# Kernel optimization log

Hardware: AMD Instinct MI355X
Metric: run time of the kernel (lower is better)

Reference implementation:

```python
import jax, jax.numpy as jnp
import numpy as np

NUM_HEADS = 16

def setup_inputs() -> dict:
    key = jax.random.key(0)
    ks = jax.random.split(key, 11)
    B, S, E, H, KV = 32, 4, 1024, NUM_HEADS, 4096
    d = E // H
    inp = {
        "x": jax.random.normal(ks[0], (B, S, E), dtype=jnp.float32),
        "cache_k": jax.random.normal(ks[1], (B, H, KV, d), dtype=jnp.float32),
        "cache_v": jax.random.normal(ks[2], (B, H, KV, d), dtype=jnp.float32),
        "Wq": jax.random.normal(ks[3], (E, E), dtype=jnp.float32) * (E ** -0.5),
        "bq": jax.random.normal(ks[4], (E,), dtype=jnp.float32) * 0.01,
        "Wk": jax.random.normal(ks[5], (E, E), dtype=jnp.float32) * (E ** -0.5),
        "bk": jax.random.normal(ks[6], (E,), dtype=jnp.float32) * 0.01,
        "Wv": jax.random.normal(ks[7], (E, E), dtype=jnp.float32) * (E ** -0.5),
        "bv": jax.random.normal(ks[8], (E,), dtype=jnp.float32) * 0.01,
        "Wo": jax.random.normal(ks[9], (E, E), dtype=jnp.float32) * (E ** -0.5),
        "bo": jax.random.normal(ks[10], (E,), dtype=jnp.float32) * 0.01,
    }
    return inp


def reference(x, cache_k, cache_v, Wq, bq, Wk, bk, Wv, bv, Wo, bo):
    B, S, E = x.shape
    H = NUM_HEADS
    d = E // H
    # torch Linear: y = x @ W.T + b
    def proj(W, b):
        return (x @ W.T + b).reshape(B, S, H, d).transpose(0, 2, 1, 3)  # [B,H,S,d]
    Q = proj(Wq, bq)
    K_new = proj(Wk, bk)
    V_new = proj(Wv, bv)
    K = jnp.concatenate([cache_k, K_new], axis=2)  # [B,H,KV+S,d]
    V = jnp.concatenate([cache_v, V_new], axis=2)
    scores = jnp.einsum("bhqd,bhkd->bhqk", Q, K) / jnp.sqrt(jnp.float32(d))
    attn = jax.nn.softmax(scores, axis=-1)
    out = jnp.einsum("bhqk,bhkd->bhqd", attn, V)  # [B,H,S,d]
    out = out.transpose(0, 2, 1, 3).reshape(B, S, E)
    return out @ Wo.T + bo
```

## Files before the change

kernel.cpp:

```cpp
#include <hip/hip_runtime.h>
#include <math.h>

#define B_   32
#define S_   4
#define H_   16
#define D_   64
#define E_   1024
#define KV_  4096
#define NBH  512
#define CS   512
#define NC   9
#define RECSZ 264

__global__ __launch_bounds__(256) void proj_kernel(
    const float* __restrict__ A, const float* __restrict__ W,
    const float* __restrict__ bias, float* __restrict__ out, int mode) {
    __shared__ float a_lds[4 * E_];
    __shared__ float res[256];
    const int t0 = blockIdx.x * 4;
    const int n0 = blockIdx.y * 64;
    const int tid = threadIdx.x;
    const int lane = tid & 63, wid = tid >> 6;
    const int sub = lane >> 4, cg = lane & 15, tsel = cg & 3;

    const float4* Ag = (const float4*)(A + (size_t)t0 * E_);
    float4* al = (float4*)a_lds;
    #pragma unroll
    for (int i = 0; i < 4; ++i) al[tid + 256 * i] = Ag[tid + 256 * i];
    __syncthreads();

    #pragma unroll
    for (int g = 0; g < 4; ++g) {
        const int r0 = n0 + wid * 16 + g * 4;
        const float4* wrow = (const float4*)(W + (size_t)r0 * E_);
        float ac0 = 0.f, ac1 = 0.f, ac2 = 0.f, ac3 = 0.f;
        #pragma unroll
        for (int kk = 0; kk < 16; ++kk) {
            float4 w4 = wrow[sub * 256 + kk * 16 + cg];
            float4 a0 = *(const float4*)&a_lds[0 * E_ + kk * 64 + cg * 4];
            float4 a1 = *(const float4*)&a_lds[1 * E_ + kk * 64 + cg * 4];
            float4 a2 = *(const float4*)&a_lds[2 * E_ + kk * 64 + cg * 4];
            float4 a3 = *(const float4*)&a_lds[3 * E_ + kk * 64 + cg * 4];
            ac0 += w4.x * a0.x + w4.y * a0.y + w4.z * a0.z + w4.w * a0.w;
            ac1 += w4.x * a1.x + w4.y * a1.y + w4.z * a1.z + w4.w * a1.w;
            ac2 += w4.x * a2.x + w4.y * a2.y + w4.z * a2.z + w4.w * a2.w;
            ac3 += w4.x * a3.x + w4.y * a3.y + w4.z * a3.z + w4.w * a3.w;
        }
        ac0 += __shfl_xor(ac0, 1); ac0 += __shfl_xor(ac0, 2);
        ac1 += __shfl_xor(ac1, 1); ac1 += __shfl_xor(ac1, 2);
        ac2 += __shfl_xor(ac2, 1); ac2 += __shfl_xor(ac2, 2);
        ac3 += __shfl_xor(ac3, 1); ac3 += __shfl_xor(ac3, 2);
        float v = (tsel & 1) ? ((tsel & 2) ? ac3 : ac1)
                             : ((tsel & 2) ? ac2 : ac0);
        v += __shfl_xor(v, 4); v += __shfl_xor(v, 8);
        if (cg < 4) res[cg * 64 + (wid * 16 + g * 4 + sub)] = v;
    }
    __syncthreads();

    const float val = res[tid] + bias[n0 + (tid & 63)];
    const int t = t0 + (tid >> 6), e = n0 + (tid & 63);
    if (mode == 0) {
        const int b = t >> 2, s = t & 3, h = e >> 6, dk = e & 63;
        out[((size_t)((b * H_ + h) * S_ + s)) * D_ + dk] = val;
    } else {
        out[(size_t)t * E_ + e] = val;
    }
}

__device__ __forceinline__ float wave_max64(float v) {
    #pragma unroll
    for (int off = 32; off > 0; off >>= 1) v = fmaxf(v, __shfl_xor(v, off));
    return v;
}

__global__ __launch_bounds__(256) void attn_partial_kernel(
    const float* __restrict__ Qw, const float* __restrict__ Kc,
    const float* __restrict__ Vc, const float* __restrict__ Kn,
    const float* __restrict__ Vn, float* __restrict__ part) {
    __shared__ float q_s[S_ * D_];
    __shared__ float ob[4][256];
    __shared__ float mw[4];
    __shared__ float lw[4][4];

    const int bh = blockIdx.x;
    const int c = blockIdx.y;
    const int tid = threadIdx.x;
    const int lane = tid & 63, wid = tid >> 6;
    const int sub = lane >> 4, cg = lane & 15, qsel = cg & 3;

    q_s[tid] = Qw[(size_t)bh * 256 + tid];
    __syncthreads();

    const float* kptr;
    const float* vptr;
    int nrows;
    if (c < 8) {
        kptr = Kc + ((size_t)bh * KV_ + c * CS) * D_;
        vptr = Vc + ((size_t)bh * KV_ + c * CS) * D_;
        nrows = CS;
    } else {
        kptr = Kn + (size_t)bh * 256;
        vptr = Vn + (size_t)bh * 256;
        nrows = S_;
    }

    const float4 q0 = *(const float4*)&q_s[0 * 64 + cg * 4];
    const float4 q1 = *(const float4*)&q_s[1 * 64 + cg * 4];
    const float4 q2 = *(const float4*)&q_s[2 * 64 + cg * 4];
    const float4 q3 = *(const float4*)&q_s[3 * 64 + cg * 4];

    const float4 z4 = make_float4(0.f, 0.f, 0.f, 0.f);
    float m_run = -INFINITY;
    float l_run = 0.f;
    float4 a0 = z4, a1 = z4, a2 = z4, a3 = z4;

    int r0 = wid * 8;
    float4 kvA = z4, vvA = z4, kvB = z4, vvB = z4;
    bool vB = false;
    if (r0 < nrows) {
        kvA = ((const float4*)(kptr + (size_t)r0 * D_))[lane];
        vvA = ((const float4*)(vptr + (size_t)r0 * D_))[lane];
        if (r0 + 4 < nrows) {
            vB = true;
            kvB = ((const float4*)(kptr + (size_t)(r0 + 4) * D_))[lane];
            vvB = ((const float4*)(vptr + (size_t)(r0 + 4) * D_))[lane];
        }
    }

    while (r0 < nrows) {
        const int rn = r0 + 32;
        float4 nkA = z4, nvA = z4, nkB = z4, nvB = z4;
        bool vBn = false;
        if (rn < nrows) {
            nkA = ((const float4*)(kptr + (size_t)rn * D_))[lane];
            nvA = ((const float4*)(vptr + (size_t)rn * D_))[lane];
            if (rn + 4 < nrows) {
                vBn = true;
                nkB = ((const float4*)(kptr + (size_t)(rn + 4) * D_))[lane];
                nvB = ((const float4*)(vptr + (size_t)(rn + 4) * D_))[lane];
            }
        }

        float pA0 = kvA.x * q0.x + kvA.y * q0.y + kvA.z * q0.z + kvA.w * q0.w;
        float pA1 = kvA.x * q1.x + kvA.y * q1.y + kvA.z * q1.z + kvA.w * q1.w;
        float pA2 = kvA.x * q2.x + kvA.y * q2.y + kvA.z * q2.z + kvA.w * q2.w;
        float pA3 = kvA.x * q3.x + kvA.y * q3.y + kvA.z * q3.z + kvA.w * q3.w;
        float pB0 = kvB.x * q0.x + kvB.y * q0.y + kvB.z * q0.z + kvB.w * q0.w;
        float pB1 = kvB.x * q1.x + kvB.y * q1.y + kvB.z * q1.z + kvB.w * q1.w;
        float pB2 = kvB.x * q2.x + kvB.y * q2.y + kvB.z * q2.z + kvB.w * q2.w;
        float pB3 = kvB.x * q3.x + kvB.y * q3.y + kvB.z * q3.z + kvB.w * q3.w;

        pA0 += __shfl_xor(pA0, 1); pA0 += __shfl_xor(pA0, 2);
        pA1 += __shfl_xor(pA1, 1); pA1 += __shfl_xor(pA1, 2);
        pA2 += __shfl_xor(pA2, 1); pA2 += __shfl_xor(pA2, 2);
        pA3 += __shfl_xor(pA3, 1); pA3 += __shfl_xor(pA3, 2);
        pB0 += __shfl_xor(pB0, 1); pB0 += __shfl_xor(pB0, 2);
        pB1 += __shfl_xor(pB1, 1); pB1 += __shfl_xor(pB1, 2);
        pB2 += __shfl_xor(pB2, 1); pB2 += __shfl_xor(pB2, 2);
        pB3 += __shfl_xor(pB3, 1); pB3 += __shfl_xor(pB3, 2);

        float sA = (qsel & 1) ? ((qsel & 2) ? pA3 : pA1)
                              : ((qsel & 2) ? pA2 : pA0);
        float sB = (qsel & 1) ? ((qsel & 2) ? pB3 : pB1)
                              : ((qsel & 2) ? pB2 : pB0);
        sA += __shfl_xor(sA, 4); sA += __shfl_xor(sA, 8);
        sB += __shfl_xor(sB, 4); sB += __shfl_xor(sB, 8);
        sA *= 0.125f;
        sB = vB ? sB * 0.125f : -INFINITY;

        const float smax = fmaxf(sA, sB);
        if (__any(smax > m_run + 8.f)) {
            const float vmax = wave_max64(smax);
            const float newm = fmaxf(m_run, vmax);
            const float scale = __expf(m_run - newm);
            a0.x *= scale; a0.y *= scale; a0.z *= scale; a0.w *= scale;
            a1.x *= scale; a1.y *= scale; a1.z *= scale; a1.w *= scale;
            a2.x *= scale; a2.y *= scale; a2.z *= scale; a2.w *= scale;
            a3.x *= scale; a3.y *= scale; a3.z *= scale; a3.w *= scale;
            l_run *= scale;
            m_run = newm;
        }
        const float pxA = __expf(sA - m_run);
        const float pxB = __expf(sB - m_run);
        l_run += (cg < 4) ? (pxA + pxB) : 0.f;

        const int srcbase = (sub << 4);
        const float pa0 = __shfl(pxA, srcbase + 0);
        const float pa1 = __shfl(pxA, srcbase + 1);
        const float pa2 = __shfl(pxA, srcbase + 2);
        const float pa3 = __shfl(pxA, srcbase + 3);
        const float pb0 = __shfl(pxB, srcbase + 0);
        const float pb1 = __shfl(pxB, srcbase + 1);
        const float pb2 = __shfl(pxB, srcbase + 2);
        const float pb3 = __shfl(pxB, srcbase + 3);

        a0.x = fmaf(pa0, vvA.x, a0.x); a0.y = fmaf(pa0, vvA.y, a0.y);
        a0.z = fmaf(pa0, vvA.z, a0.z); a0.w = fmaf(pa0, vvA.w, a0.w);
        a1.x = fmaf(pa1, vvA.x, a1.x); a1.y = fmaf(pa1, vvA.y, a1.y);
        a1.z = fmaf(pa1, vvA.z, a1.z); a1.w = fmaf(pa1, vvA.w, a1.w);
        a2.x = fmaf(pa2, vvA.x, a2.x); a2.y = fmaf(pa2, vvA.y, a2.y);
        a2.z = fmaf(pa2, vvA.z, a2.z); a2.w = fmaf(pa2, vvA.w, a2.w);
        a3.x = fmaf(pa3, vvA.x, a3.x); a3.y = fmaf(pa3, vvA.y, a3.y);
        a3.z = fmaf(pa3, vvA.z, a3.z); a3.w = fmaf(pa3, vvA.w, a3.w);

        a0.x = fmaf(pb0, vvB.x, a0.x); a0.y = fmaf(pb0, vvB.y, a0.y);
        a0.z = fmaf(pb0, vvB.z, a0.z); a0.w = fmaf(pb0, vvB.w, a0.w);
        a1.x = fmaf(pb1, vvB.x, a1.x); a1.y = fmaf(pb1, vvB.y, a1.y);
        a1.z = fmaf(pb1, vvB.z, a1.z); a1.w = fmaf(pb1, vvB.w, a1.w);
        a2.x = fmaf(pb2, vvB.x, a2.x); a2.y = fmaf(pb2, vvB.y, a2.y);
        a2.z = fmaf(pb2, vvB.z, a2.z); a2.w = fmaf(pb2, vvB.w, a2.w);
        a3.x = fmaf(pb3, vvB.x, a3.x); a3.y = fmaf(pb3, vvB.y, a3.y);
        a3.z = fmaf(pb3, vvB.z, a3.z); a3.w = fmaf(pb3, vvB.w, a3.w);

        kvA = nkA; vvA = nvA; kvB = nkB; vvB = nvB; vB = vBn;
        r0 = rn;
    }

    a0.x += __shfl_xor(a0.x, 16); a0.x += __shfl_xor(a0.x, 32);
    a0.y += __shfl_xor(a0.y, 16); a0.y += __shfl_xor(a0.y, 32);
    a0.z += __shfl_xor(a0.z, 16); a0.z += __shfl_xor(a0.z, 32);
    a0.w += __shfl_xor(a0.w, 16); a0.w += __shfl_xor(a0.w, 32);
    a1.x += __shfl_xor(a1.x, 16); a1.x += __shfl_xor(a1.x, 32);
    a1.y += __shfl_xor(a1.y, 16); a1.y += __shfl_xor(a1.y, 32);
    a1.z += __shfl_xor(a1.z, 16); a1.z += __shfl_xor(a1.z, 32);
    a1.w += __shfl_xor(a1.w, 16); a1.w += __shfl_xor(a1.w, 32);
    a2.x += __shfl_xor(a2.x, 16); a2.x += __shfl_xor(a2.x, 32);
    a2.y += __shfl_xor(a2.y, 16); a2.y += __shfl_xor(a2.y, 32);
    a2.z += __shfl_xor(a2.z, 16); a2.z += __shfl_xor(a2.z, 32);
    a2.w += __shfl_xor(a2.w, 16); a2.w += __shfl_xor(a2.w, 32);
    a3.x += __shfl_xor(a3.x, 16); a3.x += __shfl_xor(a3.x, 32);
    a3.y += __shfl_xor(a3.y, 16); a3.y += __shfl_xor(a3.y, 32);
    a3.z += __shfl_xor(a3.z, 16); a3.z += __shfl_xor(a3.z, 32);
    a3.w += __shfl_xor(a3.w, 16); a3.w += __shfl_xor(a3.w, 32);

    float l2 = l_run;
    l2 += __shfl_xor(l2, 16); l2 += __shfl_xor(l2, 32);

    if (sub == 0) {
        *(float4*)&ob[wid][0 * 64 + cg * 4] = a0;
        *(float4*)&ob[wid][1 * 64 + cg * 4] = a1;
        *(float4*)&ob[wid][2 * 64 + cg * 4] = a2;
        *(float4*)&ob[wid][3 * 64 + cg * 4] = a3;
    }
    if (lane < 4) lw[wid][lane] = l2;
    if (lane == 0) mw[wid] = m_run;
    __syncthreads();

    const float M = fmaxf(fmaxf(mw[0], mw[1]), fmaxf(mw[2], mw[3]));
    const float w0 = __expf(mw[0] - M), w1 = __expf(mw[1] - M);
    const float w2 = __expf(mw[2] - M), w3 = __expf(mw[3] - M);

    float* rec = part + ((size_t)bh * NC + c) * RECSZ;
    rec[8 + tid] = w0 * ob[0][tid] + w1 * ob[1][tid] +
                   w2 * ob[2][tid] + w3 * ob[3][tid];
    if (tid < 4) {
        rec[tid] = M;
        rec[4 + tid] = w0 * lw[0][tid] + w1 * lw[1][tid] +
                       w2 * lw[2][tid] + w3 * lw[3][tid];
    }
}

__global__ __launch_bounds__(256) void attn_combine_kernel(
    const float* __restrict__ part, float* __restrict__ attn_out) {
    const int bh = blockIdx.x;
    const int tid = threadIdx.x;
    const int q = tid >> 6, dl = tid & 63;
    const float* base = part + (size_t)bh * NC * RECSZ;

    float m = -1e30f;
    #pragma unroll
    for (int c = 0; c < NC; ++c) m = fmaxf(m, base[c * RECSZ + q]);
    float l = 0.f, o = 0.f;
    #pragma unroll
    for (int c = 0; c < NC; ++c) {
        float w = __expf(base[c * RECSZ + q] - m);
        l = fmaf(base[c * RECSZ + 4 + q], w, l);
        o = fmaf(base[c * RECSZ + 8 + tid], w, o);
    }
    const float res = o / l;
    const int b = bh >> 4, h = bh & 15;
    attn_out[((size_t)(b * S_ + q)) * E_ + h * D_ + dl] = res;
}

extern "C" void kernel_launch(void* const* d_in, const int* in_sizes, int n_in,
                              void* d_out, int out_size, void* d_ws, size_t ws_size,
                              hipStream_t stream) {
    const float* x  = (const float*)d_in[0];
    const float* ck = (const float*)d_in[1];
    const float* cv = (const float*)d_in[2];
    const float* Wq = (const float*)d_in[3];
    const float* bq = (const float*)d_in[4];
    const float* Wk = (const float*)d_in[5];
    const float* bk = (const float*)d_in[6];
    const float* Wv = (const float*)d_in[7];
    const float* bv = (const float*)d_in[8];
    const float* Wo = (const float*)d_in[9];
    const float* bo = (const float*)d_in[10];
    float* out = (float*)d_out;
    float* ws = (float*)d_ws;

    float* Qw = ws;
    float* Kn = ws + 131072;
    float* Vn = ws + 262144;
    float* part = ws + 393216;
    float* attn_out = ws + 393216 + 1216512;

    dim3 pg(32, 16), pb(256);
    hipLaunchKernelGGL(proj_kernel, pg, pb, 0, stream, x, Wq, bq, Qw, 0);
    hipLaunchKernelGGL(proj_kernel, pg, pb, 0, stream, x, Wk, bk, Kn, 0);
    hipLaunchKernelGGL(proj_kernel, pg, pb, 0, stream, x, Wv, bv, Vn, 0);
    hipLaunchKernelGGL(attn_partial_kernel, dim3(NBH, NC), dim3(256), 0, stream,
                       Qw, ck, cv, Kn, Vn, part);
    hipLaunchKernelGGL(attn_combine_kernel, dim3(NBH), dim3(256), 0, stream,
                       part, attn_out);
    hipLaunchKernelGGL(proj_kernel, pg, pb, 0, stream, attn_out, Wo, bo, out, 1);
}
```

Baseline: 251.2 us.

## Fuse QKV projections into one launch and merge combine with output projection

Batches the three Q/K/V projections into a single 3D-grid launch and folds the split-KV combine step into the output projection kernel, so the attention output never round-trips through global memory. This cuts the launch count from six to three. The GEMM core also now issues all four weight-row loads per k step in one loop, for more memory-level parallelism. In exchange, each of the 16 output-projection column blocks per batch recomputes the combine from the partials, which adds redundant reads and exp work.

```diff
diff --git a/kernel.cpp b/kernel.cpp
--- a/kernel.cpp
+++ b/kernel.cpp
@@ -12,40 +12,57 @@
 #define NC   9
 #define RECSZ 264
 
-__global__ __launch_bounds__(256) void proj_kernel(
-    const float* __restrict__ A, const float* __restrict__ W,
-    const float* __restrict__ bias, float* __restrict__ out, int mode) {
-    __shared__ float a_lds[4 * E_];
-    __shared__ float res[256];
-    const int t0 = blockIdx.x * 4;
-    const int n0 = blockIdx.y * 64;
-    const int tid = threadIdx.x;
+__device__ __forceinline__ void gemm_core(const float* __restrict__ a_lds,
+                                          const float* __restrict__ W,
+                                          int n0, int tid,
+                                          float* __restrict__ res) {
     const int lane = tid & 63, wid = tid >> 6;
     const int sub = lane >> 4, cg = lane & 15, tsel = cg & 3;
 
-    const float4* Ag = (const float4*)(A + (size_t)t0 * E_);
-    float4* al = (float4*)a_lds;
-    #pragma unroll
-    for (int i = 0; i < 4; ++i) al[tid + 256 * i] = Ag[tid + 256 * i];
-    __syncthreads();
+    float acc[4][4];
+    #pragma unroll
+    for (int g = 0; g < 4; ++g)
+        #pragma unroll
+        for (int t = 0; t < 4; ++t) acc[g][t] = 0.f;
+
+    const float4* wr0 = (const float4*)(W + (size_t)(n0 + wid * 16 + 0) * E_);
+    const float4* wr1 = (const float4*)(W + (size_t)(n0 + wid * 16 + 4) * E_);
+    const float4* wr2 = (const float4*)(W + (size_t)(n0 + wid * 16 + 8) * E_);
+    const float4* wr3 = (const float4*)(W + (size_t)(n0 + wid * 16 + 12) * E_);
+
+    #pragma unroll
+    for (int kk = 0; kk < 16; ++kk) {
+        const float4 a0 = *(const float4*)&a_lds[0 * E_ + kk * 64 + cg * 4];
+        const float4 a1 = *(const float4*)&a_lds[1 * E_ + kk * 64 + cg * 4];
+        const float4 a2 = *(const float4*)&a_lds[2 * E_ + kk * 64 + cg * 4];
+        const float4 a3 = *(const float4*)&a_lds[3 * E_ + kk * 64 + cg * 4];
+        const int wi = sub * 256 + kk * 16 + cg;
+        float4 w;
+        w = wr0[wi];
+        acc[0][0] += w.x*a0.x + w.y*a0.y + w.z*a0.z + w.w*a0.w;
+        acc[0][1] += w.x*a1.x + w.y*a1.y + w.z*a1.z + w.w*a1.w;
+        acc[0][2] += w.x*a2.x + w.y*a2.y + w.z*a2.z + w.w*a2.w;
+        acc[0][3] += w.x*a3.x + w.y*a3.y + w.z*a3.z + w.w*a3.w;
+        w = wr1[wi];
+        acc[1][0] += w.x*a0.x + w.y*a0.y + w.z*a0.z + w.w*a0.w;
+        acc[1][1] += w.x*a1.x + w.y*a1.y + w.z*a1.z + w.w*a1.w;
+        acc[1][2] += w.x*a2.x + w.y*a2.y + w.z*a2.z + w.w*a2.w;
+        acc[1][3] += w.x*a3.x + w.y*a3.y + w.z*a3.z + w.w*a3.w;
+        w = wr2[wi];
+        acc[2][0] += w.x*a0.x + w.y*a0.y + w.z*a0.z + w.w*a0.w;
+        acc[2][1] += w.x*a1.x + w.y*a1.y + w.z*a1.z + w.w*a1.w;
+        acc[2][2] += w.x*a2.x + w.y*a2.y + w.z*a2.z + w.w*a2.w;
+        acc[2][3] += w.x*a3.x + w.y*a3.y + w.z*a3.z + w.w*a3.w;
+        w = wr3[wi];
+        acc[3][0] += w.x*a0.x + w.y*a0.y + w.z*a0.z + w.w*a0.w;
+        acc[3][1] += w.x*a1.x + w.y*a1.y + w.z*a1.z + w.w*a1.w;
+        acc[3][2] += w.x*a2.x + w.y*a2.y + w.z*a2.z + w.w*a2.w;
+        acc[3][3] += w.x*a3.x + w.y*a3.y + w.z*a3.z + w.w*a3.w;
+    }
 
     #pragma unroll
     for (int g = 0; g < 4; ++g) {
-        const int r0 = n0 + wid * 16 + g * 4;
-        const float4* wrow = (const float4*)(W + (size_t)r0 * E_);
-        float ac0 = 0.f, ac1 = 0.f, ac2 = 0.f, ac3 = 0.f;
-        #pragma unroll
-        for (int kk = 0; kk < 16; ++kk) {
-            float4 w4 = wrow[sub * 256 + kk * 16 + cg];
-            float4 a0 = *(const float4*)&a_lds[0 * E_ + kk * 64 + cg * 4];
-            float4 a1 = *(const float4*)&a_lds[1 * E_ + kk * 64 + cg * 4];
-            float4 a2 = *(const float4*)&a_lds[2 * E_ + kk * 64 + cg * 4];
-            float4 a3 = *(const float4*)&a_lds[3 * E_ + kk * 64 + cg * 4];
-            ac0 += w4.x * a0.x + w4.y * a0.y + w4.z * a0.z + w4.w * a0.w;
-            ac1 += w4.x * a1.x + w4.y * a1.y + w4.z * a1.z + w4.w * a1.w;
-            ac2 += w4.x * a2.x + w4.y * a2.y + w4.z * a2.z + w4.w * a2.w;
-            ac3 += w4.x * a3.x + w4.y * a3.y + w4.z * a3.z + w4.w * a3.w;
-        }
+        float ac0 = acc[g][0], ac1 = acc[g][1], ac2 = acc[g][2], ac3 = acc[g][3];
         ac0 += __shfl_xor(ac0, 1); ac0 += __shfl_xor(ac0, 2);
         ac1 += __shfl_xor(ac1, 1); ac1 += __shfl_xor(ac1, 2);
         ac2 += __shfl_xor(ac2, 1); ac2 += __shfl_xor(ac2, 2);
@@ -55,16 +72,38 @@
         v += __shfl_xor(v, 4); v += __shfl_xor(v, 8);
         if (cg < 4) res[cg * 64 + (wid * 16 + g * 4 + sub)] = v;
     }
+}
+
+__global__ __launch_bounds__(256) void proj_qkv_kernel(
+    const float* __restrict__ x,
+    const float* __restrict__ Wq, const float* __restrict__ bq,
+    const float* __restrict__ Wk, const float* __restrict__ bk,
+    const float* __restrict__ Wv, const float* __restrict__ bv,
+    float* __restrict__ outbase) {
+    __shared__ float a_lds[4 * E_];
+    __shared__ float res[256];
+    const int t0 = blockIdx.x * 4;
+    const int n0 = blockIdx.y * 64;
+    const int z = blockIdx.z;
+    const int tid = threadIdx.x;
+
+    const float* W    = (z == 0) ? Wq : (z == 1) ? Wk : Wv;
+    const float* bias = (z == 0) ? bq : (z == 1) ? bk : bv;
+    float* out = outbase + (size_t)z * (B_ * S_ * E_);
+
+    const float4* Ag = (const float4*)(x + (size_t)t0 * E_);
+    float4* al = (float4*)a_lds;
+    #pragma unroll
+    for (int i = 0; i < 4; ++i) al[tid + 256 * i] = Ag[tid + 256 * i];
+    __syncthreads();
+
+    gemm_core(a_lds, W, n0, tid, res);
     __syncthreads();
 
     const float val = res[tid] + bias[n0 + (tid & 63)];
     const int t = t0 + (tid >> 6), e = n0 + (tid & 63);
-    if (mode == 0) {
-        const int b = t >> 2, s = t & 3, h = e >> 6, dk = e & 63;
-        out[((size_t)((b * H_ + h) * S_ + s)) * D_ + dk] = val;
-    } else {
-        out[(size_t)t * E_ + e] = val;
-    }
+    const int b = t >> 2, s = t & 3, h = e >> 6, dk = e & 63;
+    out[((size_t)((b * H_ + h) * S_ + s)) * D_ + dk] = val;
 }
 
 __device__ __forceinline__ float wave_max64(float v) {
@@ -260,26 +299,62 @@
     }
 }
 
-__global__ __launch_bounds__(256) void attn_combine_kernel(
-    const float* __restrict__ part, float* __restrict__ attn_out) {
-    const int bh = blockIdx.x;
+__global__ __launch_bounds__(256) void combine_proj_out_kernel(
+    const float* __restrict__ part, const float* __restrict__ Wo,
+    const float* __restrict__ bo, float* __restrict__ out) {
+    __shared__ float a_lds[4 * E_];
+    __shared__ float res[256];
+    __shared__ float wcoef[64][NC + 1];
+    __shared__ float linv[64];
+    const int b = blockIdx.x;
+    const int n0 = blockIdx.y * 64;
     const int tid = threadIdx.x;
-    const int q = tid >> 6, dl = tid & 63;
-    const float* base = part + (size_t)bh * NC * RECSZ;
-
-    float m = -1e30f;
-    #pragma unroll
-    for (int c = 0; c < NC; ++c) m = fmaxf(m, base[c * RECSZ + q]);
-    float l = 0.f, o = 0.f;
-    #pragma unroll
-    for (int c = 0; c < NC; ++c) {
-        float w = __expf(base[c * RECSZ + q] - m);
-        l = fmaf(base[c * RECSZ + 4 + q], w, l);
-        o = fmaf(base[c * RECSZ + 8 + tid], w, o);
-    }
-    const float res = o / l;
-    const int b = bh >> 4, h = bh & 15;
-    attn_out[((size_t)(b * S_ + q)) * E_ + h * D_ + dl] = res;
+
+    if (tid < 64) {
+        const int h = tid >> 2, s = tid & 3;
+        const float* base = part + ((size_t)(b * H_ + h) * NC) * RECSZ;
+        float m = -1e30f;
+        #pragma unroll
+        for (int c = 0; c < NC; ++c) m = fmaxf(m, base[c * RECSZ + s]);
+        float l = 0.f;
+        #pragma unroll
+        for (int c = 0; c < NC; ++c) {
+            const float w = __expf(base[c * RECSZ + s] - m);
+            wcoef[tid][c] = w;
+            l = fmaf(base[c * RECSZ + 4 + s], w, l);
+        }
+        linv[tid] = 1.f / l;
+    }
+    __syncthreads();
+
+    float4* al4 = (float4*)a_lds;
+    #pragma unroll
+    for (int i = 0; i < 4; ++i) {
+        const int idx = tid + 256 * i;
+        const int s = idx >> 8;
+        const int rest = idx & 255;
+        const int h = rest >> 4, dkg = rest & 15;
+        const float* base = part + ((size_t)(b * H_ + h) * NC) * RECSZ
+                          + 8 + s * 64 + dkg * 4;
+        float4 o = make_float4(0.f, 0.f, 0.f, 0.f);
+        #pragma unroll
+        for (int c = 0; c < NC; ++c) {
+            const float4 v = *(const float4*)(base + c * RECSZ);
+            const float w = wcoef[h * 4 + s][c];
+            o.x = fmaf(w, v.x, o.x); o.y = fmaf(w, v.y, o.y);
+            o.z = fmaf(w, v.z, o.z); o.w = fmaf(w, v.w, o.w);
+        }
+        const float li = linv[h * 4 + s];
+        o.x *= li; o.y *= li; o.z *= li; o.w *= li;
+        al4[idx] = o;
+    }
+    __syncthreads();
+
+    gemm_core(a_lds, Wo, n0, tid, res);
+    __syncthreads();
+
+    out[(size_t)(b * 4 + (tid >> 6)) * E_ + n0 + (tid & 63)] =
+        res[tid] + bo[n0 + (tid & 63)];
 }
 
 extern "C" void kernel_launch(void* const* d_in, const int* in_sizes, int n_in,
@@ -303,15 +378,11 @@
     float* Kn = ws + 131072;
     float* Vn = ws + 262144;
     float* part = ws + 393216;
-    float* attn_out = ws + 393216 + 1216512;
-
-    dim3 pg(32, 16), pb(256);
-    hipLaunchKernelGGL(proj_kernel, pg, pb, 0, stream, x, Wq, bq, Qw, 0);
-    hipLaunchKernelGGL(proj_kernel, pg, pb, 0, stream, x, Wk, bk, Kn, 0);
-    hipLaunchKernelGGL(proj_kernel, pg, pb, 0, stream, x, Wv, bv, Vn, 0);
+
+    hipLaunchKernelGGL(proj_qkv_kernel, dim3(32, 16, 3), dim3(256), 0, stream,
+                       x, Wq, bq, Wk, bk, Wv, bv, ws);
     hipLaunchKernelGGL(attn_partial_kernel, dim3(NBH, NC), dim3(256), 0, stream,
                        Qw, ck, cv, Kn, Vn, part);
-    hipLaunchKernelGGL(attn_combine_kernel, dim3(NBH), dim3(256), 0, stream,
-                       part, attn_out);
-    hipLaunchKernelGGL(proj_kernel, pg, pb, 0, stream, attn_out, Wo, bo, out, 1);
-}
+    hipLaunchKernelGGL(combine_proj_out_kernel, dim3(32, 16), dim3(256), 0, stream,
+                       part, Wo, bo, out);
+}
```

Result: slower. 273.5 us (+8.9%).
